# Kernel optimization log

Measured on AMD Instinct MI355X. Metric: run time of the kernel, lower is better.

The kernel has to match this reference:

```python
import jax, jax.numpy as jnp
import numpy as np

B, T, E, H, V = 64, 512, 512, 1024, 32000


def setup_inputs() -> dict:
    key = jax.random.key(0)
    k1, k2, k3, k4, k5 = jax.random.split(key, 5)
    scale = 1.0 / np.sqrt(H)
    return {
        "source": jax.random.randint(k1, (B, T), 0, V),
        "emb_table": jax.random.normal(k2, (V, E), dtype=jnp.float32),
        "W_ih": jax.random.normal(k3, (E, 4 * H), dtype=jnp.float32) * scale,
        "W_hh": jax.random.normal(k4, (H, 4 * H), dtype=jnp.float32) * scale,
        "b": jax.random.normal(k5, (4 * H,), dtype=jnp.float32) * scale,
    }


def reference(source, emb_table, W_ih, W_hh, b):
    # Embedding lookup: [B, T, E]
    embedded = emb_table[source]
    batch = source.shape[0]
    hidden = W_hh.shape[0]
    h0 = jnp.zeros((batch, hidden), dtype=emb_table.dtype)
    c0 = jnp.zeros((batch, hidden), dtype=emb_table.dtype)

    # Sequential LSTM cell loop over timesteps, expressed as lax.scan.
    xs = jnp.swapaxes(embedded, 0, 1)  # [T, B, E]

    def step(carry, x_t):
        h, c = carry
        z = x_t @ W_ih + h @ W_hh + b  # [B, 4H]
        i, f, g, o = jnp.split(z, 4, axis=-1)
        i = jax.nn.sigmoid(i)
        f = jax.nn.sigmoid(f)
        g = jnp.tanh(g)
        o = jax.nn.sigmoid(o)
        c_new = f * c + i * g
        h_new = o * jnp.tanh(c_new)
        return (h_new, c_new), None

    (h_T, c_T), _ = jax.lax.scan(step, (h0, c0), xs)
    return h_T, c_T
```

## Files before the change

### kernel.cpp

```cpp
#include <hip/hip_runtime.h>
#include <hip/hip_bf16.h>

#define TT 512
#define BB 64
#define EE 512
#define HH 1024

typedef __attribute__((ext_vector_type(8))) short short8;
typedef __attribute__((ext_vector_type(4))) float f32x4;
typedef __attribute__((ext_vector_type(4))) unsigned int u32x4;

#define WS_X     0
#define WS_WT    33554432
#define WS_HBUF  46137344
#define WS_FLAGS 46399488
#define WS_PROBE 48496640

static __device__ __forceinline__ unsigned short f2bf(float x) {
    unsigned int u = __float_as_uint(x);
    unsigned int r = (u + 0x7fffu + ((u >> 16) & 1u)) >> 16;
    return (unsigned short)r;
}

static __device__ __forceinline__ int fl_ld(const int* p) {
    return __hip_atomic_load(p, __ATOMIC_RELAXED, __HIP_MEMORY_SCOPE_AGENT);
}
static __device__ __forceinline__ void fl_st(int* p, int v) {
    __hip_atomic_store(p, v, __ATOMIC_RELAXED, __HIP_MEMORY_SCOPE_AGENT);
}

__global__ void embed_k(const int* __restrict__ src, const float* __restrict__ emb,
                        unsigned short* __restrict__ X) {
    int idx  = blockIdx.x * 256 + threadIdx.x;
    int base = idx * 4;
    int t = base >> 15;
    int r = base & 32767;
    int b = r >> 9;
    int e = r & 511;
    int v = src[b * TT + t];
    float4 f = *(const float4*)(emb + (size_t)v * EE + e);
    ushort4 s;
    s.x = f2bf(f.x); s.y = f2bf(f.y); s.z = f2bf(f.z); s.w = f2bf(f.w);
    *(ushort4*)(X + base) = s;
}

__global__ void wprep_k(const float* __restrict__ Wih, const float* __restrict__ Whh,
                        unsigned short* __restrict__ Wt, int* __restrict__ probe) {
    const int bid = blockIdx.x;
    const int kk  = bid % 48;
    const int ct  = bid / 48;
    const int tid = threadIdx.x;

    if (bid == 0 && tid == 0) {
        int xcd;
        asm volatile("s_getreg_b32 %0, hwreg(HW_REG_XCC_ID)" : "=s"(xcd));
        int* pr = probe;
        asm volatile("global_store_dword %0, %1, off sc0"
                     :: "v"(pr), "v"(xcd) : "memory");
        int v;
        asm volatile("global_load_dword %0, %1, off sc0\n\ts_waitcnt vmcnt(0)"
                     : "=v"(v) : "v"(pr) : "memory");
        pr[1] = v;
    }

    const int k0 = kk * 32, c0 = ct * 16;
    __shared__ float tile[32][17];
    for (int e = tid; e < 512; e += 256) {
        int kr = e >> 4, cc = e & 15;
        int k = k0 + kr;
        float v = (k < EE) ? Wih[(size_t)k * 4096 + c0 + cc]
                           : Whh[(size_t)(k - EE) * 4096 + c0 + cc];
        tile[kr][cc] = v;
    }
    __syncthreads();
    for (int e = tid; e < 512; e += 256) {
        int lane = e >> 3, j = e & 7;
        float v = tile[(lane >> 4) * 8 + j][lane & 15];
        Wt[(size_t)bid * 512 + e] = f2bf(v);
    }
}

__global__ __launch_bounds__(256, 1) void lstm_k(
    const unsigned short* __restrict__ X,
    const unsigned short* __restrict__ Wt,
    const float* __restrict__ bias,
    unsigned short* __restrict__ hbuf,
    int* __restrict__ flags,
    float* __restrict__ out)
{
    const int g        = blockIdx.x;
    const int cg       = g & 63;
    const int rg       = g >> 6;
    const int row_base = rg * 16;
    const int ubase    = cg * 16;
    const int tid  = threadIdx.x;
    const int wave = tid >> 6;
    const int lane = tid & 63;
    const int lrow = lane & 15;
    const int quad = lane >> 4;
    const int erow = tid >> 4, eu = tid & 15;

    __shared__ float zred[4][4][16][17];

    const float bi_ = bias[          ubase + eu];
    const float bf_ = bias[HH      + ubase + eu];
    const float bg_ = bias[2 * HH  + ubase + eu];
    const float bo_ = bias[3 * HH  + ubase + eu];

    short8 wr[12][4];
#pragma unroll
    for (int i = 0; i < 12; ++i) {
        const int kk = i * 4 + wave;
#pragma unroll
        for (int g4 = 0; g4 < 4; ++g4) {
            const int ct = g4 * 64 + cg;
            wr[i][g4] = *(const short8*)(Wt + ((size_t)(ct * 48 + kk)) * 512 + lane * 8);
        }
    }

    const int pidx = lane & 15;
    const int prod = 8 * (pidx >> 1) + 2 * wave + (pidx & 1);

    float creg = 0.f;

    for (int t = 0; t < TT; ++t) {
        const unsigned short* xp = X + ((size_t)(t * BB) + row_base + lrow) * EE + quad * 8;
        short8 ax[4];
#pragma unroll
        for (int i = 0; i < 4; ++i)
            asm volatile("global_load_dwordx4 %0, %1, off"
                         : "=v"(ax[i]) : "v"(xp + (i * 4 + wave) * 32) : "memory");

        if (t > 0) {
            const int* fp = &flags[(((t - 1) * 4 + rg) * 64 + prod) * 4];
            while (fl_ld(fp) == 0) { }
        }

        const unsigned short* hrow = hbuf
            + ((size_t)(((t & 1) ^ 1) * BB) + row_base + lrow) * HH + quad * 8;
        short8 ah[8];
#pragma unroll
        for (int i = 0; i < 8; ++i)
            asm volatile("global_load_dwordx4 %0, %1, off sc1"
                         : "=v"(ah[i])
                         : "v"(hrow + (size_t)((i * 4 + wave) * 32)) : "memory");

        asm volatile("s_waitcnt vmcnt(8)" ::: "memory");
        __builtin_amdgcn_sched_barrier(0);

        f32x4 acc0 = {0.f,0.f,0.f,0.f}, acc1 = {0.f,0.f,0.f,0.f};
        f32x4 acc2 = {0.f,0.f,0.f,0.f}, acc3 = {0.f,0.f,0.f,0.f};

#pragma unroll
        for (int i = 0; i < 4; ++i) {
            acc0 = __builtin_amdgcn_mfma_f32_16x16x32_bf16(ax[i], wr[i][0], acc0, 0, 0, 0);
            acc1 = __builtin_amdgcn_mfma_f32_16x16x32_bf16(ax[i], wr[i][1], acc1, 0, 0, 0);
            acc2 = __builtin_amdgcn_mfma_f32_16x16x32_bf16(ax[i], wr[i][2], acc2, 0, 0, 0);
            acc3 = __builtin_amdgcn_mfma_f32_16x16x32_bf16(ax[i], wr[i][3], acc3, 0, 0, 0);
        }

        asm volatile("s_waitcnt vmcnt(0)" ::: "memory");
        __builtin_amdgcn_sched_barrier(0);

#pragma unroll
        for (int i = 0; i < 8; ++i) {
            acc0 = __builtin_amdgcn_mfma_f32_16x16x32_bf16(ah[i], wr[i + 4][0], acc0, 0, 0, 0);
            acc1 = __builtin_amdgcn_mfma_f32_16x16x32_bf16(ah[i], wr[i + 4][1], acc1, 0, 0, 0);
            acc2 = __builtin_amdgcn_mfma_f32_16x16x32_bf16(ah[i], wr[i + 4][2], acc2, 0, 0, 0);
            acc3 = __builtin_amdgcn_mfma_f32_16x16x32_bf16(ah[i], wr[i + 4][3], acc3, 0, 0, 0);
        }

#pragma unroll
        for (int r = 0; r < 4; ++r) {
            zred[wave][0][quad * 4 + r][lrow] = acc0[r];
            zred[wave][1][quad * 4 + r][lrow] = acc1[r];
            zred[wave][2][quad * 4 + r][lrow] = acc2[r];
            zred[wave][3][quad * 4 + r][lrow] = acc3[r];
        }
        __syncthreads();

        float zi = zred[0][0][erow][eu] + zred[1][0][erow][eu]
                 + zred[2][0][erow][eu] + zred[3][0][erow][eu] + bi_;
        float zf = zred[0][1][erow][eu] + zred[1][1][erow][eu]
                 + zred[2][1][erow][eu] + zred[3][1][erow][eu] + bf_;
        float zg = zred[0][2][erow][eu] + zred[1][2][erow][eu]
                 + zred[2][2][erow][eu] + zred[3][2][erow][eu] + bg_;
        float zo = zred[0][3][erow][eu] + zred[1][3][erow][eu]
                 + zred[2][3][erow][eu] + zred[3][3][erow][eu] + bo_;
        float iv = 1.f / (1.f + __expf(-zi));
        float fv = 1.f / (1.f + __expf(-zf));
        float gv = 1.f - 2.f / (__expf(2.f * zg) + 1.f);
        float ov = 1.f / (1.f + __expf(-zo));
        float c  = fv * creg + iv * gv;
        creg = c;
        float th = 1.f - 2.f / (__expf(2.f * c) + 1.f);
        float h  = ov * th;

        if (t < TT - 1) {
            float hp1 = __shfl_xor(h, 1);
            unsigned int v01 = (unsigned int)f2bf(h) | ((unsigned int)f2bf(hp1) << 16);
            unsigned int v23 = (unsigned int)__shfl_xor((int)v01, 2);
            unsigned int v45 = (unsigned int)__shfl_xor((int)v01, 4);
            unsigned int v67 = (unsigned int)__shfl_xor((int)v23, 4);
            if ((eu & 7) == 0) {
                u32x4 pk; pk.x = v01; pk.y = v23; pk.z = v45; pk.w = v67;
                unsigned short* hw = hbuf + ((size_t)(t & 1) * BB + row_base + erow) * HH
                                   + ubase + eu;
                asm volatile("global_store_dwordx4 %0, %1, off sc1"
                             :: "v"(hw), "v"(pk) : "memory");
            }
        } else {
            out[(row_base + erow) * HH + ubase + eu] = h;
            out[BB * HH + (row_base + erow) * HH + ubase + eu] = c;
        }

        __syncthreads();
        if (t < TT - 1 && tid == 0) {
            fl_st(&flags[((t * 4 + rg) * 64 + cg) * 4], 1);
        }
    }
}

extern "C" void kernel_launch(void* const* d_in, const int* in_sizes, int n_in,
                              void* d_out, int out_size, void* d_ws, size_t ws_size,
                              hipStream_t stream) {
    const int*   src  = (const int*)d_in[0];
    const float* emb  = (const float*)d_in[1];
    const float* Wih  = (const float*)d_in[2];
    const float* Whh  = (const float*)d_in[3];
    const float* bias = (const float*)d_in[4];
    float* out = (float*)d_out;

    char* ws = (char*)d_ws;
    unsigned short* X     = (unsigned short*)(ws + WS_X);
    unsigned short* Wt    = (unsigned short*)(ws + WS_WT);
    unsigned short* hbuf  = (unsigned short*)(ws + WS_HBUF);
    int*            flags = (int*)(ws + WS_FLAGS);
    int*            probe = (int*)(ws + WS_PROBE);

    hipMemsetAsync(hbuf, 0, 2 * BB * HH * 2, stream);
    hipMemsetAsync(flags, 0, TT * 4 * 64 * 4 * 4, stream);
    embed_k<<<dim3(16384), dim3(256), 0, stream>>>(src, emb, X);
    wprep_k<<<dim3(12288), dim3(256), 0, stream>>>(Wih, Whh, Wt, probe);
    lstm_k<<<dim3(256), dim3(256), 0, stream>>>(X, Wt, bias, hbuf, flags, out);
}
```

Before: 1.750 ms.

## Replace per-step flag handshakes with poison-value polling on a 4-slot h ring

Drops the global flag array and the per-step flag store/spin. Consumers now poll the hidden-state buffer directly, retrying until no word equals a poison sentinel. A 4-deep ring is kept, with each block re-poisoning the slot two steps ahead. The z reduction buffer in shared memory is double-buffered so the trailing __syncthreads can be removed. This cuts one global round-trip and one barrier per timestep. The risk is that a real bf16 pair could equal the poison pattern, and correctness now depends on store visibility ordering and the ring depth.

```diff
diff --git a/kernel.cpp b/kernel.cpp
--- a/kernel.cpp
+++ b/kernel.cpp
@@ -13,20 +13,14 @@
 #define WS_X     0
 #define WS_WT    33554432
 #define WS_HBUF  46137344
-#define WS_FLAGS 46399488
 #define WS_PROBE 48496640
+
+#define POISON 0x7F7F7F7Fu
 
 static __device__ __forceinline__ unsigned short f2bf(float x) {
     unsigned int u = __float_as_uint(x);
     unsigned int r = (u + 0x7fffu + ((u >> 16) & 1u)) >> 16;
     return (unsigned short)r;
-}
-
-static __device__ __forceinline__ int fl_ld(const int* p) {
-    return __hip_atomic_load(p, __ATOMIC_RELAXED, __HIP_MEMORY_SCOPE_AGENT);
-}
-static __device__ __forceinline__ void fl_st(int* p, int v) {
-    __hip_atomic_store(p, v, __ATOMIC_RELAXED, __HIP_MEMORY_SCOPE_AGENT);
 }
 
 __global__ void embed_k(const int* __restrict__ src, const float* __restrict__ emb,
@@ -85,7 +79,6 @@
     const unsigned short* __restrict__ Wt,
     const float* __restrict__ bias,
     unsigned short* __restrict__ hbuf,
-    int* __restrict__ flags,
     float* __restrict__ out)
 {
     const int g        = blockIdx.x;
@@ -100,7 +93,7 @@
     const int quad = lane >> 4;
     const int erow = tid >> 4, eu = tid & 15;
 
-    __shared__ float zred[4][4][16][17];
+    __shared__ float zred[2][4][4][16][17];
 
     const float bi_ = bias[          ubase + eu];
     const float bf_ = bias[HH      + ubase + eu];
@@ -118,9 +111,6 @@
         }
     }
 
-    const int pidx = lane & 15;
-    const int prod = 8 * (pidx >> 1) + 2 * wave + (pidx & 1);
-
     float creg = 0.f;
 
     for (int t = 0; t < TT; ++t) {
@@ -131,21 +121,26 @@
             asm volatile("global_load_dwordx4 %0, %1, off"
                          : "=v"(ax[i]) : "v"(xp + (i * 4 + wave) * 32) : "memory");
 
-        if (t > 0) {
-            const int* fp = &flags[(((t - 1) * 4 + rg) * 64 + prod) * 4];
-            while (fl_ld(fp) == 0) { }
-        }
-
         const unsigned short* hrow = hbuf
-            + ((size_t)(((t & 1) ^ 1) * BB) + row_base + lrow) * HH + quad * 8;
+            + ((size_t)((t + 3) & 3) * BB + row_base + lrow) * HH + quad * 8;
         short8 ah[8];
-#pragma unroll
-        for (int i = 0; i < 8; ++i)
-            asm volatile("global_load_dwordx4 %0, %1, off sc1"
-                         : "=v"(ah[i])
-                         : "v"(hrow + (size_t)((i * 4 + wave) * 32)) : "memory");
-
-        asm volatile("s_waitcnt vmcnt(8)" ::: "memory");
+        while (true) {
+#pragma unroll
+            for (int i = 0; i < 8; ++i)
+                asm volatile("global_load_dwordx4 %0, %1, off sc1"
+                             : "=v"(ah[i])
+                             : "v"(hrow + (size_t)((i * 4 + wave) * 32)) : "memory");
+            asm volatile("s_waitcnt vmcnt(0)" ::: "memory");
+            __builtin_amdgcn_sched_barrier(0);
+            int bad = 0;
+#pragma unroll
+            for (int i = 0; i < 8; ++i) {
+                union { short8 v; unsigned int d[4]; } u; u.v = ah[i];
+                bad |= (u.d[0] == POISON) | (u.d[1] == POISON)
+                     | (u.d[2] == POISON) | (u.d[3] == POISON);
+            }
+            if (__all(bad == 0)) break;
+        }
         __builtin_amdgcn_sched_barrier(0);
 
         f32x4 acc0 = {0.f,0.f,0.f,0.f}, acc1 = {0.f,0.f,0.f,0.f};
@@ -159,9 +154,6 @@
             acc3 = __builtin_amdgcn_mfma_f32_16x16x32_bf16(ax[i], wr[i][3], acc3, 0, 0, 0);
         }
 
-        asm volatile("s_waitcnt vmcnt(0)" ::: "memory");
-        __builtin_amdgcn_sched_barrier(0);
-
 #pragma unroll
         for (int i = 0; i < 8; ++i) {
             acc0 = __builtin_amdgcn_mfma_f32_16x16x32_bf16(ah[i], wr[i + 4][0], acc0, 0, 0, 0);
@@ -170,23 +162,34 @@
             acc3 = __builtin_amdgcn_mfma_f32_16x16x32_bf16(ah[i], wr[i + 4][3], acc3, 0, 0, 0);
         }
 
+        if (lane < 8) {
+            unsigned short* pp = hbuf
+                + ((size_t)((t + 2) & 3) * BB + row_base + wave * 4 + (lane >> 1)) * HH
+                + ubase + (lane & 1) * 8;
+            u32x4 pz; pz.x = POISON; pz.y = POISON; pz.z = POISON; pz.w = POISON;
+            asm volatile("global_store_dwordx4 %0, %1, off sc1"
+                         :: "v"(pp), "v"(pz) : "memory");
+        }
+
+        const int zb = t & 1;
 #pragma unroll
         for (int r = 0; r < 4; ++r) {
-            zred[wave][0][quad * 4 + r][lrow] = acc0[r];
-            zred[wave][1][quad * 4 + r][lrow] = acc1[r];
-            zred[wave][2][quad * 4 + r][lrow] = acc2[r];
-            zred[wave][3][quad * 4 + r][lrow] = acc3[r];
-        }
-        __syncthreads();
-
-        float zi = zred[0][0][erow][eu] + zred[1][0][erow][eu]
-                 + zred[2][0][erow][eu] + zred[3][0][erow][eu] + bi_;
-        float zf = zred[0][1][erow][eu] + zred[1][1][erow][eu]
-                 + zred[2][1][erow][eu] + zred[3][1][erow][eu] + bf_;
-        float zg = zred[0][2][erow][eu] + zred[1][2][erow][eu]
-                 + zred[2][2][erow][eu] + zred[3][2][erow][eu] + bg_;
-        float zo = zred[0][3][erow][eu] + zred[1][3][erow][eu]
-                 + zred[2][3][erow][eu] + zred[3][3][erow][eu] + bo_;
+            zred[zb][wave][0][quad * 4 + r][lrow] = acc0[r];
+            zred[zb][wave][1][quad * 4 + r][lrow] = acc1[r];
+            zred[zb][wave][2][quad * 4 + r][lrow] = acc2[r];
+            zred[zb][wave][3][quad * 4 + r][lrow] = acc3[r];
+        }
+        asm volatile("s_waitcnt lgkmcnt(0)" ::: "memory");
+        asm volatile("s_barrier" ::: "memory");
+
+        float zi = zred[zb][0][0][erow][eu] + zred[zb][1][0][erow][eu]
+                 + zred[zb][2][0][erow][eu] + zred[zb][3][0][erow][eu] + bi_;
+        float zf = zred[zb][0][1][erow][eu] + zred[zb][1][1][erow][eu]
+                 + zred[zb][2][1][erow][eu] + zred[zb][3][1][erow][eu] + bf_;
+        float zg = zred[zb][0][2][erow][eu] + zred[zb][1][2][erow][eu]
+                 + zred[zb][2][2][erow][eu] + zred[zb][3][2][erow][eu] + bg_;
+        float zo = zred[zb][0][3][erow][eu] + zred[zb][1][3][erow][eu]
+                 + zred[zb][2][3][erow][eu] + zred[zb][3][3][erow][eu] + bo_;
         float iv = 1.f / (1.f + __expf(-zi));
         float fv = 1.f / (1.f + __expf(-zf));
         float gv = 1.f - 2.f / (__expf(2.f * zg) + 1.f);
@@ -204,7 +207,7 @@
             unsigned int v67 = (unsigned int)__shfl_xor((int)v23, 4);
             if ((eu & 7) == 0) {
                 u32x4 pk; pk.x = v01; pk.y = v23; pk.z = v45; pk.w = v67;
-                unsigned short* hw = hbuf + ((size_t)(t & 1) * BB + row_base + erow) * HH
+                unsigned short* hw = hbuf + ((size_t)(t & 3) * BB + row_base + erow) * HH
                                    + ubase + eu;
                 asm volatile("global_store_dwordx4 %0, %1, off sc1"
                              :: "v"(hw), "v"(pk) : "memory");
@@ -212,11 +215,6 @@
         } else {
             out[(row_base + erow) * HH + ubase + eu] = h;
             out[BB * HH + (row_base + erow) * HH + ubase + eu] = c;
-        }
-
-        __syncthreads();
-        if (t < TT - 1 && tid == 0) {
-            fl_st(&flags[((t * 4 + rg) * 64 + cg) * 4], 1);
         }
     }
 }
@@ -235,12 +233,11 @@
     unsigned short* X     = (unsigned short*)(ws + WS_X);
     unsigned short* Wt    = (unsigned short*)(ws + WS_WT);
     unsigned short* hbuf  = (unsigned short*)(ws + WS_HBUF);
-    int*            flags = (int*)(ws + WS_FLAGS);
     int*            probe = (int*)(ws + WS_PROBE);
 
-    hipMemsetAsync(hbuf, 0, 2 * BB * HH * 2, stream);
-    hipMemsetAsync(flags, 0, TT * 4 * 64 * 4 * 4, stream);
+    hipMemsetAsync(hbuf, 0x7F, (size_t)4 * BB * HH * 2, stream);
+    hipMemsetAsync((char*)hbuf + (size_t)3 * BB * HH * 2, 0, (size_t)BB * HH * 2, stream);
     embed_k<<<dim3(16384), dim3(256), 0, stream>>>(src, emb, X);
     wprep_k<<<dim3(12288), dim3(256), 0, stream>>>(Wih, Whh, Wt, probe);
-    lstm_k<<<dim3(256), dim3(256), 0, stream>>>(X, Wt, bias, hbuf, flags, out);
-}
+    lstm_k<<<dim3(256), dim3(256), 0, stream>>>(X, Wt, bias, hbuf, out);
+}
```

New measurement: 1.998 ms. 1.14x slower.

## Replace end-of-step barrier with per-wave byte flags and double-buffered LDS reduction

Applied to the files above, without the earlier changes.

Each wave now publishes its own byte of the 4-byte step flag once its h stores have drained, and consumers spin until all four bytes are set. This removes the second block-wide barrier per timestep. The LDS reduction buffer is double-buffered by timestep parity so the next step's writes cannot clobber values other waves are still reading without that barrier. It relies on byte atomic stores combining into the int word and on per-wave vmcnt waits for ordering, which may be fragile for memory visibility.

```diff
diff --git a/kernel.cpp b/kernel.cpp
--- a/kernel.cpp
+++ b/kernel.cpp
@@ -25,7 +25,7 @@
 static __device__ __forceinline__ int fl_ld(const int* p) {
     return __hip_atomic_load(p, __ATOMIC_RELAXED, __HIP_MEMORY_SCOPE_AGENT);
 }
-static __device__ __forceinline__ void fl_st(int* p, int v) {
+static __device__ __forceinline__ void fl_stb(unsigned char* p, unsigned char v) {
     __hip_atomic_store(p, v, __ATOMIC_RELAXED, __HIP_MEMORY_SCOPE_AGENT);
 }
 
@@ -100,7 +100,7 @@
     const int quad = lane >> 4;
     const int erow = tid >> 4, eu = tid & 15;
 
-    __shared__ float zred[4][4][16][17];
+    __shared__ float zred[2][4][4][16][17];
 
     const float bi_ = bias[          ubase + eu];
     const float bf_ = bias[HH      + ubase + eu];
@@ -133,7 +133,7 @@
 
         if (t > 0) {
             const int* fp = &flags[(((t - 1) * 4 + rg) * 64 + prod) * 4];
-            while (fl_ld(fp) == 0) { }
+            while (fl_ld(fp) != (int)0x01010101) { }
         }
 
         const unsigned short* hrow = hbuf
@@ -170,23 +170,25 @@
             acc3 = __builtin_amdgcn_mfma_f32_16x16x32_bf16(ah[i], wr[i + 4][3], acc3, 0, 0, 0);
         }
 
+        const int zb = t & 1;
 #pragma unroll
         for (int r = 0; r < 4; ++r) {
-            zred[wave][0][quad * 4 + r][lrow] = acc0[r];
-            zred[wave][1][quad * 4 + r][lrow] = acc1[r];
-            zred[wave][2][quad * 4 + r][lrow] = acc2[r];
-            zred[wave][3][quad * 4 + r][lrow] = acc3[r];
-        }
-        __syncthreads();
-
-        float zi = zred[0][0][erow][eu] + zred[1][0][erow][eu]
-                 + zred[2][0][erow][eu] + zred[3][0][erow][eu] + bi_;
-        float zf = zred[0][1][erow][eu] + zred[1][1][erow][eu]
-                 + zred[2][1][erow][eu] + zred[3][1][erow][eu] + bf_;
-        float zg = zred[0][2][erow][eu] + zred[1][2][erow][eu]
-                 + zred[2][2][erow][eu] + zred[3][2][erow][eu] + bg_;
-        float zo = zred[0][3][erow][eu] + zred[1][3][erow][eu]
-                 + zred[2][3][erow][eu] + zred[3][3][erow][eu] + bo_;
+            zred[zb][wave][0][quad * 4 + r][lrow] = acc0[r];
+            zred[zb][wave][1][quad * 4 + r][lrow] = acc1[r];
+            zred[zb][wave][2][quad * 4 + r][lrow] = acc2[r];
+            zred[zb][wave][3][quad * 4 + r][lrow] = acc3[r];
+        }
+        asm volatile("s_waitcnt lgkmcnt(0)" ::: "memory");
+        asm volatile("s_barrier" ::: "memory");
+
+        float zi = zred[zb][0][0][erow][eu] + zred[zb][1][0][erow][eu]
+                 + zred[zb][2][0][erow][eu] + zred[zb][3][0][erow][eu] + bi_;
+        float zf = zred[zb][0][1][erow][eu] + zred[zb][1][1][erow][eu]
+                 + zred[zb][2][1][erow][eu] + zred[zb][3][1][erow][eu] + bf_;
+        float zg = zred[zb][0][2][erow][eu] + zred[zb][1][2][erow][eu]
+                 + zred[zb][2][2][erow][eu] + zred[zb][3][2][erow][eu] + bg_;
+        float zo = zred[zb][0][3][erow][eu] + zred[zb][1][3][erow][eu]
+                 + zred[zb][2][3][erow][eu] + zred[zb][3][3][erow][eu] + bo_;
         float iv = 1.f / (1.f + __expf(-zi));
         float fv = 1.f / (1.f + __expf(-zf));
         float gv = 1.f - 2.f / (__expf(2.f * zg) + 1.f);
@@ -209,14 +211,15 @@
                 asm volatile("global_store_dwordx4 %0, %1, off sc1"
                              :: "v"(hw), "v"(pk) : "memory");
             }
+            asm volatile("s_waitcnt vmcnt(0)" ::: "memory");
+            if (lane == 0) {
+                unsigned char* fb = (unsigned char*)
+                    &flags[((t * 4 + rg) * 64 + cg) * 4];
+                fl_stb(fb + wave, (unsigned char)1);
+            }
         } else {
             out[(row_base + erow) * HH + ubase + eu] = h;
             out[BB * HH + (row_base + erow) * HH + ubase + eu] = c;
-        }
-
-        __syncthreads();
-        if (t < TT - 1 && tid == 0) {
-            fl_st(&flags[((t * 4 + rg) * 64 + cg) * 4], 1);
         }
     }
 }
```

Result: slower. 3.320 ms (+89.7%).
